# Kernel tuning notes

Hardware: AMD Instinct MI355X
Metric: run time of the kernel (lower is better)

## Reference

```python
import jax, jax.numpy as jnp
import numpy as np

# Forest topology: T full C-ary trees of depth D, processed level-by-level
# (leaves=level 0 -> roots=level D), mirroring dgl.prop_nodes_topo.
T, C, D = 4096, 2, 5
E, H = 256, 128
COUNTS = [C ** (D - d) for d in range(D + 1)]          # nodes per level in one tree
OFFS = np.cumsum([0] + COUNTS[:-1])                     # level offsets within a tree
S = int(sum(COUNTS))                                    # nodes per tree (63)
N = T * S                                               # total nodes (258048)


def _topology():
    # children indices + validity mask for one tree, then tile across the forest
    ch1 = np.zeros((S, C), np.int32)
    m1 = np.zeros((S, C), np.float32)
    for d in range(1, D + 1):
        for j in range(COUNTS[d]):
            p = OFFS[d] + j
            ch1[p] = OFFS[d - 1] + j * C + np.arange(C)
            m1[p] = 1.0
    children = (ch1[None] + (np.arange(T, dtype=np.int32) * S)[:, None, None]).reshape(N, C)
    mask = np.tile(m1, (T, 1))
    return children, mask


def _level_nodes(d):
    # global node indices at level d (static numpy, not traced)
    return (np.arange(T)[:, None] * S + OFFS[d] + np.arange(COUNTS[d])[None, :]).reshape(-1)


def setup_inputs() -> dict:
    key = jax.random.key(0)
    ks = jax.random.split(key, 6)
    children, mask = _topology()
    child_type = np.asarray(jax.random.randint(ks[0], (N, C), 0, 2), np.int32)
    sc = 0.05
    return {
        "emb": jax.random.normal(ks[1], (N, E), jnp.float32),
        "child_mask": jnp.asarray(mask),
        "W_iou": jax.random.normal(ks[2], (E, 3 * H), jnp.float32) * sc,
        "U_iou": jax.random.normal(ks[3], (2 * H, 3 * H), jnp.float32) * sc,
        "b_iou": jnp.zeros((3 * H,), jnp.float32),
        "W_f": jax.random.normal(ks[4], (E, H), jnp.float32) * sc,
        "U_f_w": jax.random.normal(ks[5], (2 * H, 2 * H), jnp.float32) * sc,
        "U_f_b": jnp.zeros((2 * H,), jnp.float32),
        "b_f": jnp.zeros((H,), jnp.float32),
        "children_idx": jnp.asarray(children),
        "child_type": jnp.asarray(child_type),
    }


def _forward(emb, child_mask, W_iou, U_iou, b_iou, W_f, U_f_w, U_f_b, b_f,
             children_idx, child_type):
    h = jnp.zeros((N, H), emb.dtype)
    c = jnp.zeros((N, H), emb.dtype)
    for d in range(D + 1):  # topological sweep; leaves reduce to zeros (no children)
        nodes = _level_nodes(d)                          # [M] static
        ch = children_idx[nodes]                         # [M, C]
        cm = child_mask[nodes]                           # [M, C]
        ty = child_type[nodes]                           # [M, C]
        h_ch = h[ch]                                     # [M, C, H] mailbox gather
        c_ch = c[ch]
        # type-masked child-hidden sums (reduce_func)
        ht0 = jnp.einsum('mc,mch->mh', jnp.where(ty == 0, cm, 0.0), h_ch)
        ht1 = jnp.einsum('mc,mch->mh', jnp.where(ty == 1, cm, 0.0), h_ch)
        h_iou = jnp.concatenate([ht0, ht1], axis=1)      # [M, 2H]
        # per-child forget gates, selected by child type
        f = (h_iou @ U_f_w + U_f_b).reshape(-1, 2, H)
        idx = jnp.broadcast_to(ty[:, :, None], ty.shape + (H,))
        f_cell = jnp.take_along_axis(f, idx, axis=1)     # [M, C, H]
        X = emb[nodes] @ W_f                             # [M, H]
        f_tk = jax.nn.sigmoid(X[:, None, :] + f_cell + b_f)
        c_cell = jnp.sum(f_tk * c_ch * cm[:, :, None], axis=1)
        # apply_node_func
        iou = emb[nodes] @ W_iou + h_iou @ U_iou + b_iou
        i, o, u = jnp.split(iou, 3, axis=1)
        c_new = jax.nn.sigmoid(i) * jnp.tanh(u) + c_cell
        h_new = jax.nn.sigmoid(o) * jnp.tanh(c_new)
        h = h.at[nodes].set(h_new)
        c = c.at[nodes].set(c_new)
    return h


def reference(emb, child_mask, W_iou, U_iou, b_iou, W_f, U_f_w, U_f_b, b_f,
              children_idx, child_type):
    return _forward(emb, child_mask, W_iou, U_iou, b_iou, W_f, U_f_w, U_f_b, b_f,
                    children_idx, child_type)
```

## Files before the change

### kernel.cpp

```cpp
#include <hip/hip_runtime.h>


typedef float f32x4 __attribute__((ext_vector_type(4)));
typedef __bf16 bf16x8 __attribute__((ext_vector_type(8)));
typedef unsigned short u16x8 __attribute__((ext_vector_type(8)));

__device__ __forceinline__ unsigned short f2bf(float x) {
  union { __bf16 b; unsigned short u; } cv;
  cv.b = (__bf16)x;
  return cv.u;
}
__device__ __forceinline__ float bf2f(unsigned short u) {
  return __uint_as_float(((unsigned int)u) << 16);
}
__device__ __forceinline__ float sigf(float x) { return 1.f / (1.f + __expf(-x)); }
__device__ __forceinline__ float tanhfast(float x) {
  return 1.f - 2.f / (__expf(2.f * x) + 1.f);
}

__global__ void prep_kernel(const float* __restrict__ Wi, const float* __restrict__ Ui,
                            const float* __restrict__ Wf, const float* __restrict__ Uf,
                            unsigned short* __restrict__ BTf) {
  int idx = blockIdx.x * 256 + threadIdx.x;
  int j = idx & 7;
  int lane = (idx >> 3) & 63;
  int ks = (idx >> 9) & 15;
  int tile = idx >> 13;
  int cl = lane & 15, kq = lane >> 4;
  int col = tile * 16 + cl;
  int k = ks * 32 + kq * 8 + j;
  float v;
  if (k < 256) {
    v = (col < 384) ? Wi[k * 384 + col] : Wf[k * 128 + ((col - 384) & 127)];
  } else {
    int kk = k & 255;
    v = (col < 384) ? Ui[kk * 384 + col] : Uf[kk * 256 + (col - 384)];
  }
  BTf[idx] = f2bf(v);
}

template <int NKS>
__device__ __forceinline__ int a_addr(int rblk, int k) {
  int mt = rblk >> 4, r = rblk & 15;
  int ks = k >> 5, kq = (k >> 3) & 3, j = k & 7;
  return (((mt * NKS + ks) * 64 + (kq << 4) + r) << 3) + j;
}

__global__ __launch_bounds__(512, 4) void fused_kernel(
    const float* __restrict__ emb, const float* __restrict__ cmask,
    const int* __restrict__ ctype,
    const unsigned short* __restrict__ BTf,
    const float* __restrict__ b_iou, const float* __restrict__ ufb,
    const float* __restrict__ bf_,
    float* __restrict__ hout, float* __restrict__ cbuf) {
  __shared__ unsigned short Alds[16384];
  __shared__ unsigned short hstash[8192];
  __shared__ float cstash[8192];

  const int tid = threadIdx.x;
  const int lane = tid & 63;
  const int w = tid >> 6;
  const int cl = lane & 15;
  const int rb = (lane >> 4) << 2;
  const int hcol = w * 16 + cl;
  const int g0 = blockIdx.x * 126;

  const unsigned short* Bw = BTf + (size_t)w * 8192 + lane * 8;

#pragma unroll
  for (int c = 0; c < 4; ++c) {
    const int ks_e = tid >> 6;
    const int lq = tid & 63;
    const int k0 = ks_e * 32 + (lq >> 4) * 8;
    const int rblk = c * 16 + (lq & 15);
    const int g = g0 + (rblk >> 5) * 63 + (rblk & 31);
    const float4 v0 = *(const float4*)&emb[(size_t)g * 256 + k0];
    const float4 v1 = *(const float4*)&emb[(size_t)g * 256 + k0 + 4];
    ushort4 p0, p1;
    p0.x = f2bf(v0.x); p0.y = f2bf(v0.y); p0.z = f2bf(v0.z); p0.w = f2bf(v0.w);
    p1.x = f2bf(v1.x); p1.y = f2bf(v1.y); p1.z = f2bf(v1.z); p1.w = f2bf(v1.w);
    unsigned short* dst = &Alds[((c * 8 + ks_e) * 64 + lq) * 8];
    *(ushort4*)dst = p0;
    *(ushort4*)(dst + 4) = p1;
  }
  __syncthreads();

  {
    f32x4 acc[4][3];
#pragma unroll
    for (int mt = 0; mt < 4; ++mt)
#pragma unroll
      for (int t = 0; t < 3; ++t) acc[mt][t] = (f32x4){0.f, 0.f, 0.f, 0.f};
    bf16x8 bA[3], bB[3];
#pragma unroll
    for (int t = 0; t < 3; ++t) bA[t] = *(const bf16x8*)&Bw[(size_t)t * 65536];
    auto step0 = [&](bf16x8(&cur)[3], bf16x8(&nxt)[3], int ks) {
      if (ks + 1 < 8) {
#pragma unroll
        for (int t = 0; t < 3; ++t)
          nxt[t] = *(const bf16x8*)&Bw[(size_t)t * 65536 + (ks + 1) * 512];
      }
      __builtin_amdgcn_s_setprio(1);
#pragma unroll
      for (int mt = 0; mt < 4; ++mt) {
        const bf16x8 a = *(const bf16x8*)&Alds[((mt * 8 + ks) * 64 + lane) << 3];
#pragma unroll
        for (int t = 0; t < 3; ++t)
          acc[mt][t] = __builtin_amdgcn_mfma_f32_16x16x32_bf16(a, cur[t], acc[mt][t], 0, 0, 0);
      }
      __builtin_amdgcn_s_setprio(0);
    };
#pragma unroll
    for (int ks2 = 0; ks2 < 4; ++ks2) {
      step0(bA, bB, 2 * ks2);
      step0(bB, bA, 2 * ks2 + 1);
    }
    const float bi = b_iou[hcol], bo = b_iou[128 + hcol], bu = b_iou[256 + hcol];
#pragma unroll
    for (int mt = 0; mt < 4; ++mt) {
#pragma unroll
      for (int r = 0; r < 4; ++r) {
        const int row = (mt << 4) + rb + r;
        const int g = g0 + (row >> 5) * 63 + (row & 31);
        const float cn = sigf(acc[mt][0][r] + bi) * tanhfast(acc[mt][2][r] + bu);
        const float hn = sigf(acc[mt][1][r] + bo) * tanhfast(cn);
        hout[(size_t)g * 128 + hcol] = hn;
        hstash[row * 128 + hcol] = f2bf(hn);
        cstash[row * 128 + hcol] = cn;
      }
    }
  }
  __syncthreads();

#pragma unroll
  for (int c = 0; c < 2; ++c) {
    const int ks_e = tid >> 6;
    const int lq = tid & 63;
    const int k0 = ks_e * 32 + (lq >> 4) * 8;
    const int rblk = c * 16 + (lq & 15);
    const int g = g0 + (rblk >> 4) * 63 + 32 + (rblk & 15);
    const float4 v0 = *(const float4*)&emb[(size_t)g * 256 + k0];
    const float4 v1 = *(const float4*)&emb[(size_t)g * 256 + k0 + 4];
    ushort4 p0, p1;
    p0.x = f2bf(v0.x); p0.y = f2bf(v0.y); p0.z = f2bf(v0.z); p0.w = f2bf(v0.w);
    p1.x = f2bf(v1.x); p1.y = f2bf(v1.y); p1.z = f2bf(v1.z); p1.w = f2bf(v1.w);
    unsigned short* dst = &Alds[((c * 16 + ks_e) * 64 + lq) * 8];
    *(ushort4*)dst = p0;
    *(ushort4*)(dst + 4) = p1;
  }
  {
    const int rblk = tid >> 4, q = tid & 15;
    const int i = rblk >> 4, j = rblk & 15;
    const int gp = g0 + i * 63 + 32 + j;
    const int ch0 = i * 32 + 2 * j, ch1 = ch0 + 1;
    const int ty0 = ctype[2 * gp], ty1 = ctype[2 * gp + 1];
    const float c0 = cmask[2 * gp], c1 = cmask[2 * gp + 1];
    const float w00 = (ty0 == 0) ? c0 : 0.f, w01 = (ty1 == 0) ? c1 : 0.f;
    const float w10 = (ty0 == 1) ? c0 : 0.f, w11 = (ty1 == 1) ? c1 : 0.f;
    const int jc = q * 8;
    const u16x8 va = *(const u16x8*)&hstash[ch0 * 128 + jc];
    const u16x8 vb = *(const u16x8*)&hstash[ch1 * 128 + jc];
    u16x8 o0, o1;
#pragma unroll
    for (int e = 0; e < 8; ++e) {
      const float fa = bf2f(va[e]), fb = bf2f(vb[e]);
      o0[e] = f2bf(w00 * fa + w01 * fb);
      o1[e] = f2bf(w10 * fa + w11 * fb);
    }
    *(u16x8*)&Alds[a_addr<16>(rblk, 256 + jc)] = o0;
    *(u16x8*)&Alds[a_addr<16>(rblk, 384 + jc)] = o1;
  }
  __syncthreads();

  {
    f32x4 acc[2][5];
#pragma unroll
    for (int mt = 0; mt < 2; ++mt)
#pragma unroll
      for (int t = 0; t < 5; ++t) acc[mt][t] = (f32x4){0.f, 0.f, 0.f, 0.f};
    bf16x8 bA[5], bB[5];
#pragma unroll
    for (int t = 0; t < 5; ++t) bA[t] = *(const bf16x8*)&Bw[(size_t)t * 65536];
    auto step1 = [&](bf16x8(&cur)[5], bf16x8(&nxt)[5], int ks) {
      if (ks + 1 < 16) {
#pragma unroll
        for (int t = 0; t < 5; ++t)
          nxt[t] = *(const bf16x8*)&Bw[(size_t)t * 65536 + (ks + 1) * 512];
      }
      __builtin_amdgcn_s_setprio(1);
#pragma unroll
      for (int mt = 0; mt < 2; ++mt) {
        const bf16x8 a = *(const bf16x8*)&Alds[((mt * 16 + ks) * 64 + lane) << 3];
#pragma unroll
        for (int t = 0; t < 5; ++t)
          acc[mt][t] = __builtin_amdgcn_mfma_f32_16x16x32_bf16(a, cur[t], acc[mt][t], 0, 0, 0);
      }
      __builtin_amdgcn_s_setprio(0);
    };
#pragma unroll
    for (int ks2 = 0; ks2 < 8; ++ks2) {
      step1(bA, bB, 2 * ks2);
      step1(bB, bA, 2 * ks2 + 1);
    }
    const float bi = b_iou[hcol], bo = b_iou[128 + hcol], bu = b_iou[256 + hcol];
    const float f0b = ufb[hcol], f1b = ufb[128 + hcol], bfv = bf_[hcol];
#pragma unroll
    for (int mt = 0; mt < 2; ++mt) {
#pragma unroll
      for (int r = 0; r < 4; ++r) {
        const int row = (mt << 4) + rb + r;
        const int i = row >> 4, j = row & 15;
        const int g = g0 + i * 63 + 32 + j;
        const int ch0 = i * 32 + 2 * j, ch1 = ch0 + 1;
        const int ty0 = ctype[2 * g], ty1 = ctype[2 * g + 1];
        const float c0v = cmask[2 * g], c1v = cmask[2 * g + 1];
        const float iv = acc[mt][0][r] + bi;
        const float ov = acc[mt][1][r] + bo;
        const float uv = acc[mt][2][r] + bu;
        const float f0 = acc[mt][3][r] + f0b;
        const float f1 = acc[mt][4][r] + f1b;
        const float fa = (ty0 == 0) ? f0 : f1;
        const float fb = (ty1 == 0) ? f0 : f1;
        const float ft0 = sigf(fa + bfv);
        const float ft1 = sigf(fb + bfv);
        const float ccell = ft0 * cstash[ch0 * 128 + hcol] * c0v +
                            ft1 * cstash[ch1 * 128 + hcol] * c1v;
        const float cn = sigf(iv) * tanhfast(uv) + ccell;
        const float hn = sigf(ov) * tanhfast(cn);
        cbuf[(size_t)g * 128 + hcol] = cn;
        hout[(size_t)g * 128 + hcol] = hn;
      }
    }
  }
}

template <bool LEAF, int MT, int WPE>
__global__ __launch_bounds__(512, WPE) void lvl_kernel(
    const float* __restrict__ emb, const float* __restrict__ cmask,
    const int* __restrict__ cidx, const int* __restrict__ ctype,
    const unsigned short* __restrict__ BTf,
    const float* __restrict__ b_iou, const float* __restrict__ ufb,
    const float* __restrict__ bf_,
    float* __restrict__ hout, float* __restrict__ cbuf,
    int lc, int cntm1, int offs) {
  constexpr int KD = LEAF ? 256 : 512;
  constexpr int NKS = KD / 32;
  constexpr int NT = LEAF ? 3 : 5;
  constexpr int ROWS = MT * 16;
  __shared__ unsigned short Alds[ROWS * KD];

  const int tid = threadIdx.x;
  const int lane = tid & 63;
  const int w = tid >> 6;
  const int m0 = blockIdx.x * ROWS;

#pragma unroll
  for (int c = 0; c < MT; ++c) {
    const int ks_e = tid >> 6;
    const int lq = tid & 63;
    const int k0 = ks_e * 32 + (lq >> 4) * 8;
    const int rblk = c * 16 + (lq & 15);
    const int m = m0 + rblk;
    const int g = ((m >> lc) * 63) + offs + (m & cntm1);
    const float4 v0 = *(const float4*)&emb[(size_t)g * 256 + k0];
    const float4 v1 = *(const float4*)&emb[(size_t)g * 256 + k0 + 4];
    ushort4 p0, p1;
    p0.x = f2bf(v0.x); p0.y = f2bf(v0.y); p0.z = f2bf(v0.z); p0.w = f2bf(v0.w);
    p1.x = f2bf(v1.x); p1.y = f2bf(v1.y); p1.z = f2bf(v1.z); p1.w = f2bf(v1.w);
    unsigned short* dst = &Alds[((c * NKS + ks_e) * 64 + lq) * 8];
    *(ushort4*)dst = p0;
    *(ushort4*)(dst + 4) = p1;
  }

  if (!LEAF) {
    constexpr int TPR = 512 / ROWS;
    constexpr int CPT = 128 / TPR;
    const int rblk = tid / TPR, q = tid % TPR;
    const int m = m0 + rblk;
    const int g = ((m >> lc) * 63) + offs + (m & cntm1);
    const int ch0 = cidx[2 * g], ch1 = cidx[2 * g + 1];
    const int ty0 = ctype[2 * g], ty1 = ctype[2 * g + 1];
    const float c0 = cmask[2 * g], c1 = cmask[2 * g + 1];
    const float w00 = (ty0 == 0) ? c0 : 0.f, w01 = (ty1 == 0) ? c1 : 0.f;
    const float w10 = (ty0 == 1) ? c0 : 0.f, w11 = (ty1 == 1) ? c1 : 0.f;
#pragma unroll
    for (int jj = 0; jj < CPT / 4; ++jj) {
      const int j = q * CPT + jj * 4;
      float4 a = *(const float4*)&hout[(size_t)ch0 * 128 + j];
      float4 b = *(const float4*)&hout[(size_t)ch1 * 128 + j];
      ushort4 p0, p1;
      p0.x = f2bf(w00 * a.x + w01 * b.x);
      p0.y = f2bf(w00 * a.y + w01 * b.y);
      p0.z = f2bf(w00 * a.z + w01 * b.z);
      p0.w = f2bf(w00 * a.w + w01 * b.w);
      p1.x = f2bf(w10 * a.x + w11 * b.x);
      p1.y = f2bf(w10 * a.y + w11 * b.y);
      p1.z = f2bf(w10 * a.z + w11 * b.z);
      p1.w = f2bf(w10 * a.w + w11 * b.w);
      *(ushort4*)&Alds[a_addr<NKS>(rblk, 256 + j)] = p0;
      *(ushort4*)&Alds[a_addr<NKS>(rblk, 384 + j)] = p1;
    }
  }
  __syncthreads();

  f32x4 acc[MT][NT];
#pragma unroll
  for (int mt = 0; mt < MT; ++mt)
#pragma unroll
    for (int t = 0; t < NT; ++t) acc[mt][t] = (f32x4){0.f, 0.f, 0.f, 0.f};

  const unsigned short* Bw = BTf + (size_t)w * 8192 + lane * 8;
  bf16x8 bA[NT], bB[NT];
#pragma unroll
  for (int t = 0; t < NT; ++t)
    bA[t] = *(const bf16x8*)&Bw[(size_t)t * 65536];

  auto step = [&](bf16x8(&cur)[NT], bf16x8(&nxt)[NT], int ks) {
    if (ks + 1 < NKS) {
#pragma unroll
      for (int t = 0; t < NT; ++t)
        nxt[t] = *(const bf16x8*)&Bw[(size_t)t * 65536 + (ks + 1) * 512];
    }
    __builtin_amdgcn_s_setprio(1);
#pragma unroll
    for (int mt = 0; mt < MT; ++mt) {
      const bf16x8 a = *(const bf16x8*)&Alds[((mt * NKS + ks) * 64 + lane) << 3];
#pragma unroll
      for (int t = 0; t < NT; ++t)
        acc[mt][t] = __builtin_amdgcn_mfma_f32_16x16x32_bf16(a, cur[t], acc[mt][t], 0, 0, 0);
    }
    __builtin_amdgcn_s_setprio(0);
  };
#pragma unroll
  for (int ks2 = 0; ks2 < NKS / 2; ++ks2) {
    step(bA, bB, 2 * ks2);
    step(bB, bA, 2 * ks2 + 1);
  }

  const int cl = lane & 15;
  const int rb = (lane >> 4) << 2;
  const int hcol = w * 16 + cl;
  const float bi = b_iou[hcol];
  const float bo = b_iou[128 + hcol];
  const float bu = b_iou[256 + hcol];
  float f0b = 0.f, f1b = 0.f, bfv = 0.f;
  if (!LEAF) { f0b = ufb[hcol]; f1b = ufb[128 + hcol]; bfv = bf_[hcol]; }

#pragma unroll
  for (int mt = 0; mt < MT; ++mt) {
#pragma unroll
    for (int r = 0; r < 4; ++r) {
      const int m = m0 + (mt << 4) + rb + r;
      const int g = ((m >> lc) * 63) + offs + (m & cntm1);
      const float iv = acc[mt][0][r] + bi;
      const float ov = acc[mt][1][r] + bo;
      const float uv = acc[mt][2][r] + bu;
      float cn;
      if (LEAF) {
        cn = sigf(iv) * tanhfast(uv);
      } else {
        const int ch0 = cidx[2 * g], ch1 = cidx[2 * g + 1];
        const int ty0 = ctype[2 * g], ty1 = ctype[2 * g + 1];
        const float c0v = cmask[2 * g], c1v = cmask[2 * g + 1];
        const float f0 = acc[mt][3][r] + f0b;
        const float f1 = acc[mt][4][r] + f1b;
        const float fa = (ty0 == 0) ? f0 : f1;
        const float fb = (ty1 == 0) ? f0 : f1;
        const float ft0 = sigf(fa + bfv);
        const float ft1 = sigf(fb + bfv);
        const float ccell = ft0 * cbuf[(size_t)ch0 * 128 + hcol] * c0v +
                            ft1 * cbuf[(size_t)ch1 * 128 + hcol] * c1v;
        cn = sigf(iv) * tanhfast(uv) + ccell;
      }
      const float hn = sigf(ov) * tanhfast(cn);
      cbuf[(size_t)g * 128 + hcol] = cn;
      hout[(size_t)g * 128 + hcol] = hn;
    }
  }
}

extern "C" void kernel_launch(void* const* d_in, const int* in_sizes, int n_in,
                              void* d_out, int out_size, void* d_ws, size_t ws_size,
                              hipStream_t stream) {
  (void)in_sizes; (void)n_in; (void)out_size; (void)ws_size;
  const float* emb   = (const float*)d_in[0];
  const float* cmask = (const float*)d_in[1];
  const float* W_iou = (const float*)d_in[2];
  const float* U_iou = (const float*)d_in[3];
  const float* b_iou = (const float*)d_in[4];
  const float* W_f   = (const float*)d_in[5];
  const float* U_f_w = (const float*)d_in[6];
  const float* U_f_b = (const float*)d_in[7];
  const float* b_f   = (const float*)d_in[8];
  const int* cidx    = (const int*)d_in[9];
  const int* ctype   = (const int*)d_in[10];
  float* hout = (float*)d_out;

  unsigned short* BTf = (unsigned short*)d_ws;
  float* cbuf = (float*)((char*)d_ws + (size_t)(1 << 20));

  prep_kernel<<<1280, 256, 0, stream>>>(W_iou, U_iou, W_f, U_f_w, BTf);

  fused_kernel<<<2048, 512, 0, stream>>>(emb, cmask, ctype, BTf, b_iou,
                                         U_f_b, b_f, hout, cbuf);
  lvl_kernel<false, 2, 4><<<1024, 512, 0, stream>>>(emb, cmask, cidx, ctype, BTf, b_iou,
                                                    U_f_b, b_f, hout, cbuf, 3, 7, 48);
  lvl_kernel<false, 2, 4><<<512, 512, 0, stream>>>(emb, cmask, cidx, ctype, BTf, b_iou,
                                                   U_f_b, b_f, hout, cbuf, 2, 3, 56);
  lvl_kernel<false, 1, 4><<<512, 512, 0, stream>>>(emb, cmask, cidx, ctype, BTf, b_iou,
                                                   U_f_b, b_f, hout, cbuf, 1, 1, 60);
  lvl_kernel<false, 1, 4><<<256, 512, 0, stream>>>(emb, cmask, cidx, ctype, BTf, b_iou,
                                                   U_f_b, b_f, hout, cbuf, 0, 0, 62);
}
```

Before: 267.0 us.

## Fuse consecutive tree levels into pair kernels with on-chip child state

Replaces the four per-level kernels with two pair kernels. Each block handles a group of whole subtrees and computes two adjacent levels in a row. The child h (stored as bf16) and c from the first level stay in shared memory for the second level, so the parent level no longer gathers them from global memory. It also cuts the number of launches, and the c write-back is skipped for the final root pair. The cost is more shared memory per block, fewer blocks for the upper levels, and extra barriers inside each block.

```diff
diff --git a/kernel.cpp b/kernel.cpp
--- a/kernel.cpp
+++ b/kernel.cpp
@@ -234,60 +234,65 @@
   }
 }
 
-template <bool LEAF, int MT, int WPE>
-__global__ __launch_bounds__(512, WPE) void lvl_kernel(
+template <int PT, int CAL, int OFFA, int OFFB, bool WRC>
+__global__ __launch_bounds__(512, 4) void pair_kernel(
     const float* __restrict__ emb, const float* __restrict__ cmask,
     const int* __restrict__ cidx, const int* __restrict__ ctype,
     const unsigned short* __restrict__ BTf,
     const float* __restrict__ b_iou, const float* __restrict__ ufb,
     const float* __restrict__ bf_,
-    float* __restrict__ hout, float* __restrict__ cbuf,
-    int lc, int cntm1, int offs) {
-  constexpr int KD = LEAF ? 256 : 512;
-  constexpr int NKS = KD / 32;
-  constexpr int NT = LEAF ? 3 : 5;
-  constexpr int ROWS = MT * 16;
-  __shared__ unsigned short Alds[ROWS * KD];
+    float* __restrict__ hout, float* __restrict__ cbuf) {
+  constexpr int CA = 1 << CAL;
+  constexpr int RA = PT * CA;
+  constexpr int RB = RA / 2;
+  static_assert(RA == 32 && RB == 16, "pair geometry");
+  __shared__ unsigned short Alds[RA * 512];
+  __shared__ unsigned short hstash[RA * 128];
+  __shared__ float cstash[RA * 128];
 
   const int tid = threadIdx.x;
   const int lane = tid & 63;
   const int w = tid >> 6;
-  const int m0 = blockIdx.x * ROWS;
-
-#pragma unroll
-  for (int c = 0; c < MT; ++c) {
-    const int ks_e = tid >> 6;
-    const int lq = tid & 63;
-    const int k0 = ks_e * 32 + (lq >> 4) * 8;
-    const int rblk = c * 16 + (lq & 15);
-    const int m = m0 + rblk;
-    const int g = ((m >> lc) * 63) + offs + (m & cntm1);
+  const int cl = lane & 15;
+  const int rb = (lane >> 4) << 2;
+  const int hcol = w * 16 + cl;
+  const int t0 = blockIdx.x * PT;
+
+  const unsigned short* Bw = BTf + (size_t)w * 8192 + lane * 8;
+  const float bi = b_iou[hcol], bo = b_iou[128 + hcol], bu = b_iou[256 + hcol];
+  const float f0b = ufb[hcol], f1b = ufb[128 + hcol], bfv = bf_[hcol];
+
+#pragma unroll
+  for (int it = 0; it < 2; ++it) {
+    const int f = it * 512 + tid;
+    const int rblk = f >> 5, sub = f & 31;
+    const int i = rblk >> CAL, j = rblk & (CA - 1);
+    const int g = (t0 + i) * 63 + OFFA + j;
+    const int k0 = sub * 8;
     const float4 v0 = *(const float4*)&emb[(size_t)g * 256 + k0];
     const float4 v1 = *(const float4*)&emb[(size_t)g * 256 + k0 + 4];
     ushort4 p0, p1;
     p0.x = f2bf(v0.x); p0.y = f2bf(v0.y); p0.z = f2bf(v0.z); p0.w = f2bf(v0.w);
     p1.x = f2bf(v1.x); p1.y = f2bf(v1.y); p1.z = f2bf(v1.z); p1.w = f2bf(v1.w);
-    unsigned short* dst = &Alds[((c * NKS + ks_e) * 64 + lq) * 8];
+    unsigned short* dst = &Alds[a_addr<16>(rblk, k0)];
     *(ushort4*)dst = p0;
     *(ushort4*)(dst + 4) = p1;
   }
-
-  if (!LEAF) {
-    constexpr int TPR = 512 / ROWS;
-    constexpr int CPT = 128 / TPR;
-    const int rblk = tid / TPR, q = tid % TPR;
-    const int m = m0 + rblk;
-    const int g = ((m >> lc) * 63) + offs + (m & cntm1);
+  {
+    const int rblk = tid >> 4, q = tid & 15;
+    const int i = rblk >> CAL, j = rblk & (CA - 1);
+    const int g = (t0 + i) * 63 + OFFA + j;
     const int ch0 = cidx[2 * g], ch1 = cidx[2 * g + 1];
     const int ty0 = ctype[2 * g], ty1 = ctype[2 * g + 1];
     const float c0 = cmask[2 * g], c1 = cmask[2 * g + 1];
     const float w00 = (ty0 == 0) ? c0 : 0.f, w01 = (ty1 == 0) ? c1 : 0.f;
     const float w10 = (ty0 == 1) ? c0 : 0.f, w11 = (ty1 == 1) ? c1 : 0.f;
-#pragma unroll
-    for (int jj = 0; jj < CPT / 4; ++jj) {
-      const int j = q * CPT + jj * 4;
-      float4 a = *(const float4*)&hout[(size_t)ch0 * 128 + j];
-      float4 b = *(const float4*)&hout[(size_t)ch1 * 128 + j];
+    const int jv = q * 8;
+#pragma unroll
+    for (int jj = 0; jj < 2; ++jj) {
+      const int jc = jv + jj * 4;
+      float4 a = *(const float4*)&hout[(size_t)ch0 * 128 + jc];
+      float4 b = *(const float4*)&hout[(size_t)ch1 * 128 + jc];
       ushort4 p0, p1;
       p0.x = f2bf(w00 * a.x + w01 * b.x);
       p0.y = f2bf(w00 * a.y + w01 * b.y);
@@ -297,71 +302,55 @@
       p1.y = f2bf(w10 * a.y + w11 * b.y);
       p1.z = f2bf(w10 * a.z + w11 * b.z);
       p1.w = f2bf(w10 * a.w + w11 * b.w);
-      *(ushort4*)&Alds[a_addr<NKS>(rblk, 256 + j)] = p0;
-      *(ushort4*)&Alds[a_addr<NKS>(rblk, 384 + j)] = p1;
-    }
-  }
-  __syncthreads();
-
-  f32x4 acc[MT][NT];
-#pragma unroll
-  for (int mt = 0; mt < MT; ++mt)
-#pragma unroll
-    for (int t = 0; t < NT; ++t) acc[mt][t] = (f32x4){0.f, 0.f, 0.f, 0.f};
-
-  const unsigned short* Bw = BTf + (size_t)w * 8192 + lane * 8;
-  bf16x8 bA[NT], bB[NT];
-#pragma unroll
-  for (int t = 0; t < NT; ++t)
-    bA[t] = *(const bf16x8*)&Bw[(size_t)t * 65536];
-
-  auto step = [&](bf16x8(&cur)[NT], bf16x8(&nxt)[NT], int ks) {
-    if (ks + 1 < NKS) {
-#pragma unroll
-      for (int t = 0; t < NT; ++t)
-        nxt[t] = *(const bf16x8*)&Bw[(size_t)t * 65536 + (ks + 1) * 512];
-    }
-    __builtin_amdgcn_s_setprio(1);
-#pragma unroll
-    for (int mt = 0; mt < MT; ++mt) {
-      const bf16x8 a = *(const bf16x8*)&Alds[((mt * NKS + ks) * 64 + lane) << 3];
-#pragma unroll
-      for (int t = 0; t < NT; ++t)
-        acc[mt][t] = __builtin_amdgcn_mfma_f32_16x16x32_bf16(a, cur[t], acc[mt][t], 0, 0, 0);
-    }
-    __builtin_amdgcn_s_setprio(0);
-  };
-#pragma unroll
-  for (int ks2 = 0; ks2 < NKS / 2; ++ks2) {
-    step(bA, bB, 2 * ks2);
-    step(bB, bA, 2 * ks2 + 1);
-  }
-
-  const int cl = lane & 15;
-  const int rb = (lane >> 4) << 2;
-  const int hcol = w * 16 + cl;
-  const float bi = b_iou[hcol];
-  const float bo = b_iou[128 + hcol];
-  const float bu = b_iou[256 + hcol];
-  float f0b = 0.f, f1b = 0.f, bfv = 0.f;
-  if (!LEAF) { f0b = ufb[hcol]; f1b = ufb[128 + hcol]; bfv = bf_[hcol]; }
-
-#pragma unroll
-  for (int mt = 0; mt < MT; ++mt) {
-#pragma unroll
-    for (int r = 0; r < 4; ++r) {
-      const int m = m0 + (mt << 4) + rb + r;
-      const int g = ((m >> lc) * 63) + offs + (m & cntm1);
-      const float iv = acc[mt][0][r] + bi;
-      const float ov = acc[mt][1][r] + bo;
-      const float uv = acc[mt][2][r] + bu;
-      float cn;
-      if (LEAF) {
-        cn = sigf(iv) * tanhfast(uv);
-      } else {
+      *(ushort4*)&Alds[a_addr<16>(rblk, 256 + jc)] = p0;
+      *(ushort4*)&Alds[a_addr<16>(rblk, 384 + jc)] = p1;
+    }
+  }
+  __syncthreads();
+
+  {
+    f32x4 acc[2][5];
+#pragma unroll
+    for (int mt = 0; mt < 2; ++mt)
+#pragma unroll
+      for (int t = 0; t < 5; ++t) acc[mt][t] = (f32x4){0.f, 0.f, 0.f, 0.f};
+    bf16x8 bA[5], bB[5];
+#pragma unroll
+    for (int t = 0; t < 5; ++t) bA[t] = *(const bf16x8*)&Bw[(size_t)t * 65536];
+    auto stepA = [&](bf16x8(&cur)[5], bf16x8(&nxt)[5], int ks) {
+      if (ks + 1 < 16) {
+#pragma unroll
+        for (int t = 0; t < 5; ++t)
+          nxt[t] = *(const bf16x8*)&Bw[(size_t)t * 65536 + (ks + 1) * 512];
+      }
+      __builtin_amdgcn_s_setprio(1);
+#pragma unroll
+      for (int mt = 0; mt < 2; ++mt) {
+        const bf16x8 a = *(const bf16x8*)&Alds[((mt * 16 + ks) * 64 + lane) << 3];
+#pragma unroll
+        for (int t = 0; t < 5; ++t)
+          acc[mt][t] = __builtin_amdgcn_mfma_f32_16x16x32_bf16(a, cur[t], acc[mt][t], 0, 0, 0);
+      }
+      __builtin_amdgcn_s_setprio(0);
+    };
+#pragma unroll
+    for (int ks2 = 0; ks2 < 8; ++ks2) {
+      stepA(bA, bB, 2 * ks2);
+      stepA(bB, bA, 2 * ks2 + 1);
+    }
+#pragma unroll
+    for (int mt = 0; mt < 2; ++mt) {
+#pragma unroll
+      for (int r = 0; r < 4; ++r) {
+        const int row = (mt << 4) + rb + r;
+        const int i = row >> CAL, j = row & (CA - 1);
+        const int g = (t0 + i) * 63 + OFFA + j;
         const int ch0 = cidx[2 * g], ch1 = cidx[2 * g + 1];
         const int ty0 = ctype[2 * g], ty1 = ctype[2 * g + 1];
         const float c0v = cmask[2 * g], c1v = cmask[2 * g + 1];
+        const float iv = acc[mt][0][r] + bi;
+        const float ov = acc[mt][1][r] + bo;
+        const float uv = acc[mt][2][r] + bu;
         const float f0 = acc[mt][3][r] + f0b;
         const float f1 = acc[mt][4][r] + f1b;
         const float fa = (ty0 == 0) ? f0 : f1;
@@ -370,11 +359,103 @@
         const float ft1 = sigf(fb + bfv);
         const float ccell = ft0 * cbuf[(size_t)ch0 * 128 + hcol] * c0v +
                             ft1 * cbuf[(size_t)ch1 * 128 + hcol] * c1v;
-        cn = sigf(iv) * tanhfast(uv) + ccell;
-      }
+        const float cn = sigf(iv) * tanhfast(uv) + ccell;
+        const float hn = sigf(ov) * tanhfast(cn);
+        hout[(size_t)g * 128 + hcol] = hn;
+        hstash[row * 128 + hcol] = f2bf(hn);
+        cstash[row * 128 + hcol] = cn;
+      }
+    }
+  }
+  __syncthreads();
+
+  {
+    const int f = tid;
+    const int rblk = f >> 5, sub = f & 31;
+    const int iB = rblk >> (CAL - 1), jB = rblk & ((CA / 2) - 1);
+    const int g = (t0 + iB) * 63 + OFFB + jB;
+    const int k0 = sub * 8;
+    const float4 v0 = *(const float4*)&emb[(size_t)g * 256 + k0];
+    const float4 v1 = *(const float4*)&emb[(size_t)g * 256 + k0 + 4];
+    ushort4 p0, p1;
+    p0.x = f2bf(v0.x); p0.y = f2bf(v0.y); p0.z = f2bf(v0.z); p0.w = f2bf(v0.w);
+    p1.x = f2bf(v1.x); p1.y = f2bf(v1.y); p1.z = f2bf(v1.z); p1.w = f2bf(v1.w);
+    unsigned short* dst = &Alds[a_addr<16>(rblk, k0)];
+    *(ushort4*)dst = p0;
+    *(ushort4*)(dst + 4) = p1;
+  }
+  if (tid < RB * 16) {
+    const int rblk = tid >> 4, q = tid & 15;
+    const int iB = rblk >> (CAL - 1), jB = rblk & ((CA / 2) - 1);
+    const int g = (t0 + iB) * 63 + OFFB + jB;
+    const int chb = iB * CA + 2 * jB;
+    const int ty0 = ctype[2 * g], ty1 = ctype[2 * g + 1];
+    const float c0 = cmask[2 * g], c1 = cmask[2 * g + 1];
+    const float w00 = (ty0 == 0) ? c0 : 0.f, w01 = (ty1 == 0) ? c1 : 0.f;
+    const float w10 = (ty0 == 1) ? c0 : 0.f, w11 = (ty1 == 1) ? c1 : 0.f;
+    const int jc = q * 8;
+    const u16x8 va = *(const u16x8*)&hstash[chb * 128 + jc];
+    const u16x8 vb = *(const u16x8*)&hstash[(chb + 1) * 128 + jc];
+    u16x8 o0, o1;
+#pragma unroll
+    for (int e = 0; e < 8; ++e) {
+      const float fa = bf2f(va[e]), fb = bf2f(vb[e]);
+      o0[e] = f2bf(w00 * fa + w01 * fb);
+      o1[e] = f2bf(w10 * fa + w11 * fb);
+    }
+    *(u16x8*)&Alds[a_addr<16>(rblk, 256 + jc)] = o0;
+    *(u16x8*)&Alds[a_addr<16>(rblk, 384 + jc)] = o1;
+  }
+  __syncthreads();
+
+  {
+    f32x4 acc[1][5];
+#pragma unroll
+    for (int t = 0; t < 5; ++t) acc[0][t] = (f32x4){0.f, 0.f, 0.f, 0.f};
+    bf16x8 bA[5], bB[5];
+#pragma unroll
+    for (int t = 0; t < 5; ++t) bA[t] = *(const bf16x8*)&Bw[(size_t)t * 65536];
+    auto stepB = [&](bf16x8(&cur)[5], bf16x8(&nxt)[5], int ks) {
+      if (ks + 1 < 16) {
+#pragma unroll
+        for (int t = 0; t < 5; ++t)
+          nxt[t] = *(const bf16x8*)&Bw[(size_t)t * 65536 + (ks + 1) * 512];
+      }
+      __builtin_amdgcn_s_setprio(1);
+      const bf16x8 a = *(const bf16x8*)&Alds[((ks)*64 + lane) << 3];
+#pragma unroll
+      for (int t = 0; t < 5; ++t)
+        acc[0][t] = __builtin_amdgcn_mfma_f32_16x16x32_bf16(a, cur[t], acc[0][t], 0, 0, 0);
+      __builtin_amdgcn_s_setprio(0);
+    };
+#pragma unroll
+    for (int ks2 = 0; ks2 < 8; ++ks2) {
+      stepB(bA, bB, 2 * ks2);
+      stepB(bB, bA, 2 * ks2 + 1);
+    }
+#pragma unroll
+    for (int r = 0; r < 4; ++r) {
+      const int row = rb + r;
+      const int iB = row >> (CAL - 1), jB = row & ((CA / 2) - 1);
+      const int g = (t0 + iB) * 63 + OFFB + jB;
+      const int chb = iB * CA + 2 * jB;
+      const int ty0 = ctype[2 * g], ty1 = ctype[2 * g + 1];
+      const float c0v = cmask[2 * g], c1v = cmask[2 * g + 1];
+      const float iv = acc[0][0][r] + bi;
+      const float ov = acc[0][1][r] + bo;
+      const float uv = acc[0][2][r] + bu;
+      const float f0 = acc[0][3][r] + f0b;
+      const float f1 = acc[0][4][r] + f1b;
+      const float fa = (ty0 == 0) ? f0 : f1;
+      const float fb = (ty1 == 0) ? f0 : f1;
+      const float ft0 = sigf(fa + bfv);
+      const float ft1 = sigf(fb + bfv);
+      const float ccell = ft0 * cstash[chb * 128 + hcol] * c0v +
+                          ft1 * cstash[(chb + 1) * 128 + hcol] * c1v;
+      const float cn = sigf(iv) * tanhfast(uv) + ccell;
       const float hn = sigf(ov) * tanhfast(cn);
-      cbuf[(size_t)g * 128 + hcol] = cn;
       hout[(size_t)g * 128 + hcol] = hn;
+      if (WRC) cbuf[(size_t)g * 128 + hcol] = cn;
     }
   }
 }
@@ -403,12 +484,8 @@
 
   fused_kernel<<<2048, 512, 0, stream>>>(emb, cmask, ctype, BTf, b_iou,
                                          U_f_b, b_f, hout, cbuf);
-  lvl_kernel<false, 2, 4><<<1024, 512, 0, stream>>>(emb, cmask, cidx, ctype, BTf, b_iou,
-                                                    U_f_b, b_f, hout, cbuf, 3, 7, 48);
-  lvl_kernel<false, 2, 4><<<512, 512, 0, stream>>>(emb, cmask, cidx, ctype, BTf, b_iou,
-                                                   U_f_b, b_f, hout, cbuf, 2, 3, 56);
-  lvl_kernel<false, 1, 4><<<512, 512, 0, stream>>>(emb, cmask, cidx, ctype, BTf, b_iou,
-                                                   U_f_b, b_f, hout, cbuf, 1, 1, 60);
-  lvl_kernel<false, 1, 4><<<256, 512, 0, stream>>>(emb, cmask, cidx, ctype, BTf, b_iou,
-                                                   U_f_b, b_f, hout, cbuf, 0, 0, 62);
-}
+  pair_kernel<4, 3, 48, 56, true><<<1024, 512, 0, stream>>>(
+      emb, cmask, cidx, ctype, BTf, b_iou, U_f_b, b_f, hout, cbuf);
+  pair_kernel<16, 1, 60, 62, false><<<256, 512, 0, stream>>>(
+      emb, cmask, cidx, ctype, BTf, b_iou, U_f_b, b_f, hout, cbuf);
+}
```

Measured after the change: 431.0 us. +61.4%, slower.

## Fuse tree level 2 into the fused leaf kernel via LDS stash

Applied to the files above, without the earlier changes.

Extends the fused kernel so that, after computing level-1 nodes, it writes their h (as bf16) and c into shared memory and immediately computes level-2 nodes in the same block. This removes a separate level kernel launch, along with the global round trip of level-1 h/c and the gather of children. Level-1 children's c values are preloaded into registers behind a scheduling barrier so the stash can be overwritten safely. The cost is extra LDS traffic, added register pressure, and a serial extra phase per block.

```diff
diff --git a/kernel.cpp b/kernel.cpp
--- a/kernel.cpp
+++ b/kernel.cpp
@@ -202,6 +202,20 @@
       step1(bA, bB, 2 * ks2);
       step1(bB, bA, 2 * ks2 + 1);
     }
+    float lc0[2][4], lc1[2][4];
+#pragma unroll
+    for (int mt = 0; mt < 2; ++mt) {
+#pragma unroll
+      for (int r = 0; r < 4; ++r) {
+        const int row = (mt << 4) + rb + r;
+        const int i = row >> 4, j = row & 15;
+        const int ch0 = i * 32 + 2 * j;
+        lc0[mt][r] = cstash[ch0 * 128 + hcol];
+        lc1[mt][r] = cstash[(ch0 + 1) * 128 + hcol];
+      }
+    }
+    __builtin_amdgcn_sched_barrier(0);
+
     const float bi = b_iou[hcol], bo = b_iou[128 + hcol], bu = b_iou[256 + hcol];
     const float f0b = ufb[hcol], f1b = ufb[128 + hcol], bfv = bf_[hcol];
 #pragma unroll
@@ -211,7 +225,6 @@
         const int row = (mt << 4) + rb + r;
         const int i = row >> 4, j = row & 15;
         const int g = g0 + i * 63 + 32 + j;
-        const int ch0 = i * 32 + 2 * j, ch1 = ch0 + 1;
         const int ty0 = ctype[2 * g], ty1 = ctype[2 * g + 1];
         const float c0v = cmask[2 * g], c1v = cmask[2 * g + 1];
         const float iv = acc[mt][0][r] + bi;
@@ -223,13 +236,104 @@
         const float fb = (ty1 == 0) ? f0 : f1;
         const float ft0 = sigf(fa + bfv);
         const float ft1 = sigf(fb + bfv);
-        const float ccell = ft0 * cstash[ch0 * 128 + hcol] * c0v +
-                            ft1 * cstash[ch1 * 128 + hcol] * c1v;
+        const float ccell = ft0 * lc0[mt][r] * c0v + ft1 * lc1[mt][r] * c1v;
         const float cn = sigf(iv) * tanhfast(uv) + ccell;
         const float hn = sigf(ov) * tanhfast(cn);
-        cbuf[(size_t)g * 128 + hcol] = cn;
         hout[(size_t)g * 128 + hcol] = hn;
-      }
+        hstash[row * 128 + hcol] = f2bf(hn);
+        cstash[row * 128 + hcol] = cn;
+      }
+    }
+  }
+  __syncthreads();
+
+  {
+    const int rblk = tid >> 5, sub = tid & 31;
+    const int g = g0 + (rblk >> 3) * 63 + 48 + (rblk & 7);
+    const int k0 = sub * 8;
+    const float4 v0 = *(const float4*)&emb[(size_t)g * 256 + k0];
+    const float4 v1 = *(const float4*)&emb[(size_t)g * 256 + k0 + 4];
+    ushort4 p0, p1;
+    p0.x = f2bf(v0.x); p0.y = f2bf(v0.y); p0.z = f2bf(v0.z); p0.w = f2bf(v0.w);
+    p1.x = f2bf(v1.x); p1.y = f2bf(v1.y); p1.z = f2bf(v1.z); p1.w = f2bf(v1.w);
+    unsigned short* dst = &Alds[a_addr<16>(rblk, k0)];
+    *(ushort4*)dst = p0;
+    *(ushort4*)(dst + 4) = p1;
+  }
+  if (tid < 256) {
+    const int rblk = tid >> 4, q = tid & 15;
+    const int i = rblk >> 3, j = rblk & 7;
+    const int gp = g0 + i * 63 + 48 + j;
+    const int ch0 = i * 16 + 2 * j, ch1 = ch0 + 1;
+    const int ty0 = ctype[2 * gp], ty1 = ctype[2 * gp + 1];
+    const float c0 = cmask[2 * gp], c1 = cmask[2 * gp + 1];
+    const float w00 = (ty0 == 0) ? c0 : 0.f, w01 = (ty1 == 0) ? c1 : 0.f;
+    const float w10 = (ty0 == 1) ? c0 : 0.f, w11 = (ty1 == 1) ? c1 : 0.f;
+    const int jc = q * 8;
+    const u16x8 va = *(const u16x8*)&hstash[ch0 * 128 + jc];
+    const u16x8 vb = *(const u16x8*)&hstash[ch1 * 128 + jc];
+    u16x8 o0, o1;
+#pragma unroll
+    for (int e = 0; e < 8; ++e) {
+      const float fa = bf2f(va[e]), fb = bf2f(vb[e]);
+      o0[e] = f2bf(w00 * fa + w01 * fb);
+      o1[e] = f2bf(w10 * fa + w11 * fb);
+    }
+    *(u16x8*)&Alds[a_addr<16>(rblk, 256 + jc)] = o0;
+    *(u16x8*)&Alds[a_addr<16>(rblk, 384 + jc)] = o1;
+  }
+  __syncthreads();
+
+  {
+    f32x4 acc[1][5];
+#pragma unroll
+    for (int t = 0; t < 5; ++t) acc[0][t] = (f32x4){0.f, 0.f, 0.f, 0.f};
+    bf16x8 bA[5], bB[5];
+#pragma unroll
+    for (int t = 0; t < 5; ++t) bA[t] = *(const bf16x8*)&Bw[(size_t)t * 65536];
+    auto step2 = [&](bf16x8(&cur)[5], bf16x8(&nxt)[5], int ks) {
+      if (ks + 1 < 16) {
+#pragma unroll
+        for (int t = 0; t < 5; ++t)
+          nxt[t] = *(const bf16x8*)&Bw[(size_t)t * 65536 + (ks + 1) * 512];
+      }
+      __builtin_amdgcn_s_setprio(1);
+      const bf16x8 a = *(const bf16x8*)&Alds[(ks * 64 + lane) << 3];
+#pragma unroll
+      for (int t = 0; t < 5; ++t)
+        acc[0][t] = __builtin_amdgcn_mfma_f32_16x16x32_bf16(a, cur[t], acc[0][t], 0, 0, 0);
+      __builtin_amdgcn_s_setprio(0);
+    };
+#pragma unroll
+    for (int ks2 = 0; ks2 < 8; ++ks2) {
+      step2(bA, bB, 2 * ks2);
+      step2(bB, bA, 2 * ks2 + 1);
+    }
+    const float bi = b_iou[hcol], bo = b_iou[128 + hcol], bu = b_iou[256 + hcol];
+    const float f0b = ufb[hcol], f1b = ufb[128 + hcol], bfv = bf_[hcol];
+#pragma unroll
+    for (int r = 0; r < 4; ++r) {
+      const int row = rb + r;
+      const int i = row >> 3, j = row & 7;
+      const int g = g0 + i * 63 + 48 + j;
+      const int ch0 = i * 16 + 2 * j, ch1 = ch0 + 1;
+      const int ty0 = ctype[2 * g], ty1 = ctype[2 * g + 1];
+      const float c0v = cmask[2 * g], c1v = cmask[2 * g + 1];
+      const float iv = acc[0][0][r] + bi;
+      const float ov = acc[0][1][r] + bo;
+      const float uv = acc[0][2][r] + bu;
+      const float f0 = acc[0][3][r] + f0b;
+      const float f1 = acc[0][4][r] + f1b;
+      const float fa = (ty0 == 0) ? f0 : f1;
+      const float fb = (ty1 == 0) ? f0 : f1;
+      const float ft0 = sigf(fa + bfv);
+      const float ft1 = sigf(fb + bfv);
+      const float ccell = ft0 * cstash[ch0 * 128 + hcol] * c0v +
+                          ft1 * cstash[ch1 * 128 + hcol] * c1v;
+      const float cn = sigf(iv) * tanhfast(uv) + ccell;
+      const float hn = sigf(ov) * tanhfast(cn);
+      cbuf[(size_t)g * 128 + hcol] = cn;
+      hout[(size_t)g * 128 + hcol] = hn;
     }
   }
 }
@@ -403,8 +507,6 @@
 
   fused_kernel<<<2048, 512, 0, stream>>>(emb, cmask, ctype, BTf, b_iou,
                                          U_f_b, b_f, hout, cbuf);
-  lvl_kernel<false, 2, 4><<<1024, 512, 0, stream>>>(emb, cmask, cidx, ctype, BTf, b_iou,
-                                                    U_f_b, b_f, hout, cbuf, 3, 7, 48);
   lvl_kernel<false, 2, 4><<<512, 512, 0, stream>>>(emb, cmask, cidx, ctype, BTf, b_iou,
                                                    U_f_b, b_f, hout, cbuf, 2, 3, 56);
   lvl_kernel<false, 1, 4><<<512, 512, 0, stream>>>(emb, cmask, cidx, ctype, BTf, b_iou,
```

New measurement: 399.8 us. 1.5x slower.
